# Kernel optimization log

Hardware: AMD Instinct MI355X
Metric: run time of the kernel (lower is better)

Reference implementation:

```python
import jax, jax.numpy as jnp
import numpy as np

B, T, N, C_IN, C_OUT, CHEB_K, ST_EMB = 8, 12, 2048, 64, 64, 2, 64


def setup_inputs() -> dict:
    key = jax.random.key(0)
    ks = jax.random.split(key, 9)
    inv = 1.0 / np.sqrt(ST_EMB)
    return {
        "x": jax.random.normal(ks[0], (B, T, N, C_IN), dtype=jnp.float32),
        "adj": jax.random.uniform(ks[1], (N, N), dtype=jnp.float32),
        "st_emb": jax.random.normal(ks[2], (T, 1, ST_EMB), dtype=jnp.float32),
        "weights": jax.random.normal(ks[3], (CHEB_K, C_IN, C_OUT), dtype=jnp.float32) * 0.02,
        "bias": jax.random.normal(ks[4], (C_OUT,), dtype=jnp.float32) * 0.02,
        "W1": jax.random.uniform(ks[5], (ST_EMB, 32), minval=-inv, maxval=inv, dtype=jnp.float32),
        "b1": jax.random.uniform(ks[6], (32,), minval=-inv, maxval=inv, dtype=jnp.float32),
        "W2": jax.random.uniform(ks[7], (32, 1), minval=-1/np.sqrt(32), maxval=1/np.sqrt(32), dtype=jnp.float32),
        "b2": jax.random.uniform(ks[8], (1,), minval=-1/np.sqrt(32), maxval=1/np.sqrt(32), dtype=jnp.float32),
    }


def reference(x, adj, st_emb, weights, bias, W1, b1, W2, b2):
    # lambda MLP: Linear -> ReLU -> Linear, then 1 + relu(.)
    h = jax.nn.relu(st_emb @ W1 + b1)            # [T,1,32]
    lam = 1.0 + jax.nn.relu(h @ W2 + b2)         # [T,1,1]
    c1 = (2.0 * lam - 2.0) / lam                 # [T,1,1] diagonal-scale coefficient
    c2 = 2.0 / lam                               # [T,1,1]
    # identity support einsum == per-time diagonal scaling of x
    x_g1 = c1[None] * x                          # [B,T,N,C]
    # adjacency support: scale factored out of the N x N contraction
    x_g2 = c2[None] * jnp.einsum('nm,btmc->btnc', adj, x)  # [B,T,N,C]
    x_g = jnp.stack([x_g1, x_g2], axis=3)        # [B,T,N,K,C]
    return jnp.einsum('btnki,kio->btno', x_g, weights) + bias
```

## Files before the change

kernel.cpp:

```cpp
#include <hip/hip_runtime.h>
#include <hip/hip_bf16.h>

#define B_ 8
#define T_ 12
#define N_ 2048
#define C_ 64
#define BM 128
#define BK 64

typedef __attribute__((ext_vector_type(4))) float f32x4;
typedef __attribute__((ext_vector_type(4))) __bf16 bf16x4;
typedef __attribute__((ext_vector_type(8))) __bf16 bf16x8;

#define GAS __attribute__((address_space(1)))
#define LAS __attribute__((address_space(3)))

static __device__ __forceinline__ void gld_lds16(const void* g, void* l) {
    __builtin_amdgcn_global_load_lds((const GAS void*)g, (LAS void*)l, 16, 0, 0);
}

#define WS_CBUF 0
#define WS_WTB  1024
#define WS_ADJB 32768
#define WS_XT   (32768 + 8388608)
#define WS_NEED ((size_t)(WS_XT) + 25165824)

__global__ void lam_kernel(const float* __restrict__ st, const float* __restrict__ W1,
                           const float* __restrict__ b1, const float* __restrict__ W2,
                           const float* __restrict__ b2, float* __restrict__ cbuf) {
    const int t = threadIdx.x >> 5;
    const int h = threadIdx.x & 31;
    if (t >= T_) return;
    float acc = b1[h];
    #pragma unroll 8
    for (int e = 0; e < 64; ++e) acc += st[t * 64 + e] * W1[e * 32 + h];
    float hv = fmaxf(acc, 0.f) * W2[h];
    #pragma unroll
    for (int off = 16; off; off >>= 1) hv += __shfl_down(hv, off, 32);
    if (h == 0) {
        float lam = 1.f + fmaxf(hv + b2[0], 0.f);
        cbuf[t]      = 2.f - 2.f / lam;
        cbuf[T_ + t] = 2.f / lam;
    }
}

__global__ void lamw_kernel(const float* __restrict__ st, const float* __restrict__ W1,
                            const float* __restrict__ b1, const float* __restrict__ W2,
                            const float* __restrict__ b2, const float* __restrict__ weights,
                            float* __restrict__ cbuf, __bf16* __restrict__ WtB) {
    const int t = threadIdx.x >> 5;
    const int h = threadIdx.x & 31;
    if (t < T_) {
        float acc = b1[h];
        #pragma unroll 8
        for (int e = 0; e < 64; ++e) acc += st[t * 64 + e] * W1[e * 32 + h];
        float hv = fmaxf(acc, 0.f) * W2[h];
        #pragma unroll
        for (int off = 16; off; off >>= 1) hv += __shfl_down(hv, off, 32);
        if (h == 0) {
            float lam = 1.f + fmaxf(hv + b2[0], 0.f);
            cbuf[t]      = 2.f - 2.f / lam;
            cbuf[T_ + t] = 2.f / lam;
        }
    }
    for (int e = threadIdx.x; e < 64 * 128; e += 512) {
        int o = e >> 7, k = e & 127;
        float v = (k < 64) ? weights[4096 + k * 64 + o] : weights[(k - 64) * 64 + o];
        WtB[o * 128 + k] = (__bf16)v;
    }
}

__global__ void cvt_adj(const float* __restrict__ adj, __bf16* __restrict__ adjb) {
    const int i = (blockIdx.x * 256 + threadIdx.x) * 8;
    const float4 f0 = *(const float4*)&adj[i];
    const float4 f1 = *(const float4*)&adj[i + 4];
    bf16x8 h = { (__bf16)f0.x, (__bf16)f0.y, (__bf16)f0.z, (__bf16)f0.w,
                 (__bf16)f1.x, (__bf16)f1.y, (__bf16)f1.z, (__bf16)f1.w };
    *(bf16x8*)&adjb[i] = h;
}

__global__ void cvt_x(const float* __restrict__ x, __bf16* __restrict__ xT) {
    __shared__ __align__(16) __bf16 t[64][72];
    const int bt = blockIdx.y, n0 = blockIdx.x * 64;
    const int tid = threadIdx.x;
    {
        const int r = tid >> 2, c0 = (tid & 3) * 16;
        const float* src = x + ((size_t)bt * N_ + n0 + r) * C_ + c0;
        #pragma unroll
        for (int i = 0; i < 4; ++i) {
            float4 f = *(const float4*)(src + 4 * i);
            t[c0 + 4 * i + 0][r] = (__bf16)f.x;
            t[c0 + 4 * i + 1][r] = (__bf16)f.y;
            t[c0 + 4 * i + 2][r] = (__bf16)f.z;
            t[c0 + 4 * i + 3][r] = (__bf16)f.w;
        }
    }
    __syncthreads();
    {
        const int c = tid >> 2, nf = (tid & 3) * 16;
        __bf16* dst = xT + ((size_t)bt * C_ + c) * N_ + n0 + nf;
        *(bf16x8*)(dst)     = *(const bf16x8*)&t[c][nf];
        *(bf16x8*)(dst + 8) = *(const bf16x8*)&t[c][nf + 8];
    }
}

__global__ __launch_bounds__(256, 3) void dgcn_main2(
    const __bf16* __restrict__ adjb, const __bf16* __restrict__ xT,
    const float* __restrict__ x, const __bf16* __restrict__ WtB,
    const float* __restrict__ bias, const float* __restrict__ cbuf,
    float* __restrict__ out)
{
    __shared__ __align__(16) __bf16 smem[24576];
    char* sb = (char*)smem;

    const int m0  = blockIdx.x * BM;
    const int btg = blockIdx.y;
    const int tid = threadIdx.x;
    const int l   = tid & 63, w = tid >> 6;
    const int wr  = w >> 1, wc = w & 1;
    const int lr  = l & 15, lk = l >> 4;

    #pragma unroll
    for (int i = 0; i < 4; ++i) {
        int s = (w * 4 + i) * 64 + l;
        int o = s >> 4, j = s & 15;
        *(bf16x8*)(sb + 32768 + s * 16) = *(const bf16x8*)(WtB + o * 128 + 8 * (j ^ (o & 7)));
    }

    const __bf16* srcA[4];
    const __bf16* srcB[4];
    #pragma unroll
    for (int i = 0; i < 4; ++i) {
        int s = (w * 4 + i) * 64 + l;
        int r = s >> 3, j = s & 7;
        srcA[i] = adjb + (size_t)(m0 + r) * N_ + 8 * (j ^ (r & 7));
        int bb = s >> 9, c = (s >> 3) & 63;
        srcB[i] = xT + ((size_t)(btg * 2 + bb) * C_ + c) * N_ + 8 * (j ^ (c & 7));
    }

    f32x4 acc[4][4] = {};

    for (int kt = 0; kt < N_ / BK; ++kt) {
        __syncthreads();
        #pragma unroll
        for (int i = 0; i < 4; ++i) {
            gld_lds16(srcA[i], sb + (w * 4 + i) * 1024);
            gld_lds16(srcB[i], sb + 16384 + (w * 4 + i) * 1024);
            srcA[i] += BK;
            srcB[i] += BK;
        }
        __syncthreads();
        #pragma unroll
        for (int ks = 0; ks < 2; ++ks) {
            const int kb = ks * 64 + lk * 16;
            bf16x8 a[4];
            #pragma unroll
            for (int mi = 0; mi < 4; ++mi) {
                int rr = wr * 64 + mi * 16 + lr;
                a[mi] = *(const bf16x8*)(sb + rr * 128 + (kb ^ ((rr & 7) << 4)));
            }
            #pragma unroll
            for (int nj = 0; nj < 4; ++nj) {
                int cc = nj * 16 + lr;
                bf16x8 b = *(const bf16x8*)(sb + 16384 + wc * 8192 + cc * 128 + (kb ^ ((cc & 7) << 4)));
                #pragma unroll
                for (int mi = 0; mi < 4; ++mi)
                    acc[mi][nj] = __builtin_amdgcn_mfma_f32_16x16x32_bf16(a[mi], b, acc[mi][nj], 0, 0, 0);
            }
        }
    }

    #pragma unroll
    for (int bb = 0; bb < 2; ++bb) {
        const int btA = btg * 2 + bb;
        const int tloc = btA % T_;
        const float c1 = cbuf[tloc];
        const float c2 = cbuf[T_ + tloc];
        __syncthreads();
        if (wc == bb) {
            #pragma unroll
            for (int mi = 0; mi < 4; ++mi)
                #pragma unroll
                for (int nj = 0; nj < 4; ++nj)
                    #pragma unroll
                    for (int q = 0; q < 4; ++q) {
                        int row = wr * 64 + mi * 16 + lk * 4 + q;
                        int colb = (nj * 16 + lr) * 2;
                        *(__bf16*)(sb + row * 256 + (colb ^ ((row & 7) << 4))) =
                            (__bf16)(c2 * acc[mi][nj][q]);
                    }
        }
        {
            int row = w * 32 + (l >> 1);
            int c0 = (l & 1) * 32;
            const float* xs = x + ((size_t)btA * N_ + m0 + row) * C_ + c0;
            #pragma unroll
            for (int i = 0; i < 4; ++i) {
                float4 f0 = *(const float4*)(xs + 8 * i);
                float4 f1 = *(const float4*)(xs + 8 * i + 4);
                bf16x8 h = { (__bf16)(c1 * f0.x), (__bf16)(c1 * f0.y),
                             (__bf16)(c1 * f0.z), (__bf16)(c1 * f0.w),
                             (__bf16)(c1 * f1.x), (__bf16)(c1 * f1.y),
                             (__bf16)(c1 * f1.z), (__bf16)(c1 * f1.w) };
                int colb = 128 + c0 * 2 + 16 * i;
                *(bf16x8*)(sb + row * 256 + (colb ^ ((row & 7) << 4))) = h;
            }
        }
        __syncthreads();
        f32x4 oacc[2][4] = {};
        #pragma unroll
        for (int ks = 0; ks < 4; ++ks) {
            const int kb = ks * 64 + lk * 16;
            bf16x8 ea[2];
            #pragma unroll
            for (int mi2 = 0; mi2 < 2; ++mi2) {
                int row = w * 32 + mi2 * 16 + lr;
                ea[mi2] = *(const bf16x8*)(sb + row * 256 + (kb ^ ((row & 7) << 4)));
            }
            #pragma unroll
            for (int nj = 0; nj < 4; ++nj) {
                int o = nj * 16 + lr;
                bf16x8 bw = *(const bf16x8*)(sb + 32768 + o * 256 + (kb ^ ((o & 7) << 4)));
                oacc[0][nj] = __builtin_amdgcn_mfma_f32_16x16x32_bf16(ea[0], bw, oacc[0][nj], 0, 0, 0);
                oacc[1][nj] = __builtin_amdgcn_mfma_f32_16x16x32_bf16(ea[1], bw, oacc[1][nj], 0, 0, 0);
            }
        }
        float* ob = out + (size_t)btA * N_ * C_;
        #pragma unroll
        for (int nj = 0; nj < 4; ++nj) {
            const float bv = bias[nj * 16 + lr];
            #pragma unroll
            for (int mi2 = 0; mi2 < 2; ++mi2)
                #pragma unroll
                for (int q = 0; q < 4; ++q) {
                    int row = w * 32 + mi2 * 16 + lk * 4 + q;
                    ob[(size_t)(m0 + row) * C_ + nj * 16 + lr] = oacc[mi2][nj][q] + bv;
                }
        }
    }
}

#define LDM 72
#define LDE 136
__global__ __launch_bounds__(256, 3) void dgcn_fb(
    const float* __restrict__ x, const float* __restrict__ adj,
    const float* __restrict__ weights, const float* __restrict__ bias,
    const float* __restrict__ cbuf, float* __restrict__ out)
{
    __shared__ __align__(16) __bf16 smem[BM * LDE];
    __shared__ __align__(16) __bf16 Wt[64 * LDE];
    __bf16* As = smem;
    __bf16* Bs = smem + BM * LDM;
    __bf16* E  = smem;

    const int mtile = blockIdx.x;
    const int bt    = blockIdx.y;
    const int tloc  = bt % T_;
    const int m0    = mtile * BM;
    const int tid   = threadIdx.x;
    const int lane  = tid & 63;
    const int w     = tid >> 6;

    const float c1 = cbuf[tloc];
    const float c2 = cbuf[T_ + tloc];
    const float* xbt = x + (size_t)bt * N_ * C_;

    for (int e = tid; e < 2 * 64 * 64; e += 256) {
        int kk = e >> 6, o = e & 63;
        float v = (kk < 64) ? weights[4096 + kk * 64 + o] : weights[(kk - 64) * 64 + o];
        Wt[o * LDE + kk] = (__bf16)v;
    }

    f32x4 acc[2][4] = {};
    const int c4 = tid & 15;
    const int rg = tid >> 4;
    const int lr = lane & 15;
    const int lk = lane >> 4;

    for (int kt = 0; kt < N_ / BK; ++kt) {
        const int k0 = kt * BK;
        __syncthreads();
        #pragma unroll
        for (int j = 0; j < 8; ++j) {
            const int r = rg + 16 * j;
            const float4 f = *(const float4*)&adj[(size_t)(m0 + r) * N_ + k0 + 4 * c4];
            bf16x4 h = { (__bf16)f.x, (__bf16)f.y, (__bf16)f.z, (__bf16)f.w };
            *(bf16x4*)&As[r * LDM + 4 * c4] = h;
        }
        #pragma unroll
        for (int j = 0; j < 4; ++j) {
            const int k  = (tid & 15) + 16 * j;
            const int c0 = 4 * (tid >> 4);
            const float4 f = *(const float4*)&xbt[(size_t)(k0 + k) * C_ + c0];
            Bs[(c0 + 0) * LDM + k] = (__bf16)f.x;
            Bs[(c0 + 1) * LDM + k] = (__bf16)f.y;
            Bs[(c0 + 2) * LDM + k] = (__bf16)f.z;
            Bs[(c0 + 3) * LDM + k] = (__bf16)f.w;
        }
        __syncthreads();
        #pragma unroll
        for (int ks = 0; ks < 2; ++ks) {
            bf16x8 a0 = *(const bf16x8*)&As[(w * 32 +  0 + lr) * LDM + ks * 32 + lk * 8];
            bf16x8 a1 = *(const bf16x8*)&As[(w * 32 + 16 + lr) * LDM + ks * 32 + lk * 8];
            #pragma unroll
            for (int nj = 0; nj < 4; ++nj) {
                bf16x8 b = *(const bf16x8*)&Bs[(nj * 16 + lr) * LDM + ks * 32 + lk * 8];
                acc[0][nj] = __builtin_amdgcn_mfma_f32_16x16x32_bf16(a0, b, acc[0][nj], 0, 0, 0);
                acc[1][nj] = __builtin_amdgcn_mfma_f32_16x16x32_bf16(a1, b, acc[1][nj], 0, 0, 0);
            }
        }
    }
    __syncthreads();

    #pragma unroll
    for (int j = 0; j < 8; ++j) {
        const int r = rg + 16 * j;
        const float4 f = *(const float4*)&xbt[(size_t)(m0 + r) * C_ + 4 * c4];
        bf16x4 h = { (__bf16)(c1 * f.x), (__bf16)(c1 * f.y), (__bf16)(c1 * f.z), (__bf16)(c1 * f.w) };
        *(bf16x4*)&E[r * LDE + 64 + 4 * c4] = h;
    }
    #pragma unroll
    for (int mi = 0; mi < 2; ++mi)
        #pragma unroll
        for (int nj = 0; nj < 4; ++nj)
            #pragma unroll
            for (int q = 0; q < 4; ++q) {
                const int row = w * 32 + mi * 16 + lk * 4 + q;
                const int col = nj * 16 + lr;
                E[row * LDE + col] = (__bf16)(c2 * acc[mi][nj][q]);
            }
    __syncthreads();

    f32x4 oacc[2][4] = {};
    #pragma unroll
    for (int ks = 0; ks < 4; ++ks) {
        bf16x8 a0 = *(const bf16x8*)&E[(w * 32 +  0 + lr) * LDE + ks * 32 + lk * 8];
        bf16x8 a1 = *(const bf16x8*)&E[(w * 32 + 16 + lr) * LDE + ks * 32 + lk * 8];
        #pragma unroll
        for (int nj = 0; nj < 4; ++nj) {
            bf16x8 bw = *(const bf16x8*)&Wt[(nj * 16 + lr) * LDE + ks * 32 + lk * 8];
            oacc[0][nj] = __builtin_amdgcn_mfma_f32_16x16x32_bf16(a0, bw, oacc[0][nj], 0, 0, 0);
            oacc[1][nj] = __builtin_amdgcn_mfma_f32_16x16x32_bf16(a1, bw, oacc[1][nj], 0, 0, 0);
        }
    }
    float* obt = out + (size_t)bt * N_ * C_;
    #pragma unroll
    for (int nj = 0; nj < 4; ++nj) {
        const float bv = bias[nj * 16 + lr];
        #pragma unroll
        for (int mi = 0; mi < 2; ++mi)
            #pragma unroll
            for (int q = 0; q < 4; ++q) {
                const int row = w * 32 + mi * 16 + lk * 4 + q;
                obt[(size_t)(m0 + row) * C_ + nj * 16 + lr] = oacc[mi][nj][q] + bv;
            }
    }
}

extern "C" void kernel_launch(void* const* d_in, const int* in_sizes, int n_in,
                              void* d_out, int out_size, void* d_ws, size_t ws_size,
                              hipStream_t stream) {
    const float* x       = (const float*)d_in[0];
    const float* adj     = (const float*)d_in[1];
    const float* st_emb  = (const float*)d_in[2];
    const float* weights = (const float*)d_in[3];
    const float* bias    = (const float*)d_in[4];
    const float* W1      = (const float*)d_in[5];
    const float* b1      = (const float*)d_in[6];
    const float* W2      = (const float*)d_in[7];
    const float* b2      = (const float*)d_in[8];
    float* out = (float*)d_out;
    char* ws = (char*)d_ws;
    float* cbuf = (float*)(ws + WS_CBUF);

    if (ws_size >= WS_NEED) {
        __bf16* WtB  = (__bf16*)(ws + WS_WTB);
        __bf16* adjb = (__bf16*)(ws + WS_ADJB);
        __bf16* xT   = (__bf16*)(ws + WS_XT);
        lamw_kernel<<<1, 512, 0, stream>>>(st_emb, W1, b1, W2, b2, weights, cbuf, WtB);
        cvt_adj<<<N_ * N_ / (256 * 8), 256, 0, stream>>>(adj, adjb);
        cvt_x<<<dim3(N_ / 64, B_ * T_), 256, 0, stream>>>(x, xT);
        dgcn_main2<<<dim3(N_ / BM, B_ * T_ / 2), 256, 0, stream>>>(adjb, xT, x, WtB, bias, cbuf, out);
    } else {
        lam_kernel<<<1, 384, 0, stream>>>(st_emb, W1, b1, W2, b2, cbuf);
        dgcn_fb<<<dim3(N_ / BM, B_ * T_), 256, 0, stream>>>(x, adj, weights, bias, cbuf, out);
    }
}
```

Before: 90.05 us.

## Double-buffer LDS tiles in main GEMM and fuse adj/x conversion kernels

The main adjacency GEMM now double-buffers its LDS tiles: the next K-tile's async global-to-LDS loads are issued before computing on the current buffer, which removes one barrier per iteration and overlaps loads with MFMA work. LDS grows from 48KB to 64KB, so launch bounds drop to 2 blocks per CU and the output weights are read straight from global memory instead of being staged in LDS. The two conversion kernels for adj and x are merged into a single launch to cut launch overhead. A single barrier per iteration with async LDS loads may leave a write-after-read hazard unless the wait semantics cover it, and occupancy is lower.

```diff
diff --git a/kernel.cpp b/kernel.cpp
--- a/kernel.cpp
+++ b/kernel.cpp
@@ -70,19 +70,21 @@
     }
 }
 
-__global__ void cvt_adj(const float* __restrict__ adj, __bf16* __restrict__ adjb) {
-    const int i = (blockIdx.x * 256 + threadIdx.x) * 8;
-    const float4 f0 = *(const float4*)&adj[i];
-    const float4 f1 = *(const float4*)&adj[i + 4];
-    bf16x8 h = { (__bf16)f0.x, (__bf16)f0.y, (__bf16)f0.z, (__bf16)f0.w,
-                 (__bf16)f1.x, (__bf16)f1.y, (__bf16)f1.z, (__bf16)f1.w };
-    *(bf16x8*)&adjb[i] = h;
-}
-
-__global__ void cvt_x(const float* __restrict__ x, __bf16* __restrict__ xT) {
+__global__ void cvt_fused(const float* __restrict__ x, __bf16* __restrict__ xT,
+                          const float* __restrict__ adj, __bf16* __restrict__ adjb) {
+    const int bid = blockIdx.x;
+    const int tid = threadIdx.x;
+    if (bid >= 3072) {
+        const size_t i = ((size_t)(bid - 3072) * 256 + tid) * 8;
+        const float4 f0 = *(const float4*)&adj[i];
+        const float4 f1 = *(const float4*)&adj[i + 4];
+        bf16x8 h = { (__bf16)f0.x, (__bf16)f0.y, (__bf16)f0.z, (__bf16)f0.w,
+                     (__bf16)f1.x, (__bf16)f1.y, (__bf16)f1.z, (__bf16)f1.w };
+        *(bf16x8*)&adjb[i] = h;
+        return;
+    }
     __shared__ __align__(16) __bf16 t[64][72];
-    const int bt = blockIdx.y, n0 = blockIdx.x * 64;
-    const int tid = threadIdx.x;
+    const int bt = bid >> 5, n0 = (bid & 31) * 64;
     {
         const int r = tid >> 2, c0 = (tid & 3) * 16;
         const float* src = x + ((size_t)bt * N_ + n0 + r) * C_ + c0;
@@ -104,13 +106,13 @@
     }
 }
 
-__global__ __launch_bounds__(256, 3) void dgcn_main2(
+__global__ __launch_bounds__(256, 2) void dgcn_main2(
     const __bf16* __restrict__ adjb, const __bf16* __restrict__ xT,
     const float* __restrict__ x, const __bf16* __restrict__ WtB,
     const float* __restrict__ bias, const float* __restrict__ cbuf,
     float* __restrict__ out)
 {
-    __shared__ __align__(16) __bf16 smem[24576];
+    __shared__ __align__(16) __bf16 smem[32768];
     char* sb = (char*)smem;
 
     const int m0  = blockIdx.x * BM;
@@ -120,13 +122,6 @@
     const int wr  = w >> 1, wc = w & 1;
     const int lr  = l & 15, lk = l >> 4;
 
-    #pragma unroll
-    for (int i = 0; i < 4; ++i) {
-        int s = (w * 4 + i) * 64 + l;
-        int o = s >> 4, j = s & 15;
-        *(bf16x8*)(sb + 32768 + s * 16) = *(const bf16x8*)(WtB + o * 128 + 8 * (j ^ (o & 7)));
-    }
-
     const __bf16* srcA[4];
     const __bf16* srcB[4];
     #pragma unroll
@@ -140,16 +135,26 @@
 
     f32x4 acc[4][4] = {};
 
+    #pragma unroll
+    for (int i = 0; i < 4; ++i) {
+        gld_lds16(srcA[i], sb + (w * 4 + i) * 1024);
+        gld_lds16(srcB[i], sb + 16384 + (w * 4 + i) * 1024);
+    }
+
+    int sel = 0;
     for (int kt = 0; kt < N_ / BK; ++kt) {
         __syncthreads();
-        #pragma unroll
-        for (int i = 0; i < 4; ++i) {
-            gld_lds16(srcA[i], sb + (w * 4 + i) * 1024);
-            gld_lds16(srcB[i], sb + 16384 + (w * 4 + i) * 1024);
-            srcA[i] += BK;
-            srcB[i] += BK;
-        }
-        __syncthreads();
+        if (kt < N_ / BK - 1) {
+            const int wo = (sel ^ 1) * 32768;
+            #pragma unroll
+            for (int i = 0; i < 4; ++i) {
+                srcA[i] += BK;
+                srcB[i] += BK;
+                gld_lds16(srcA[i], sb + wo + (w * 4 + i) * 1024);
+                gld_lds16(srcB[i], sb + wo + 16384 + (w * 4 + i) * 1024);
+            }
+        }
+        const char* base = sb + sel * 32768;
         #pragma unroll
         for (int ks = 0; ks < 2; ++ks) {
             const int kb = ks * 64 + lk * 16;
@@ -157,17 +162,18 @@
             #pragma unroll
             for (int mi = 0; mi < 4; ++mi) {
                 int rr = wr * 64 + mi * 16 + lr;
-                a[mi] = *(const bf16x8*)(sb + rr * 128 + (kb ^ ((rr & 7) << 4)));
+                a[mi] = *(const bf16x8*)(base + rr * 128 + (kb ^ ((rr & 7) << 4)));
             }
             #pragma unroll
             for (int nj = 0; nj < 4; ++nj) {
                 int cc = nj * 16 + lr;
-                bf16x8 b = *(const bf16x8*)(sb + 16384 + wc * 8192 + cc * 128 + (kb ^ ((cc & 7) << 4)));
+                bf16x8 b = *(const bf16x8*)(base + 16384 + wc * 8192 + cc * 128 + (kb ^ ((cc & 7) << 4)));
                 #pragma unroll
                 for (int mi = 0; mi < 4; ++mi)
                     acc[mi][nj] = __builtin_amdgcn_mfma_f32_16x16x32_bf16(a[mi], b, acc[mi][nj], 0, 0, 0);
             }
         }
+        sel ^= 1;
     }
 
     #pragma unroll
@@ -220,7 +226,7 @@
             #pragma unroll
             for (int nj = 0; nj < 4; ++nj) {
                 int o = nj * 16 + lr;
-                bf16x8 bw = *(const bf16x8*)(sb + 32768 + o * 256 + (kb ^ ((o & 7) << 4)));
+                bf16x8 bw = *(const bf16x8*)(WtB + o * 128 + ks * 32 + lk * 8);
                 oacc[0][nj] = __builtin_amdgcn_mfma_f32_16x16x32_bf16(ea[0], bw, oacc[0][nj], 0, 0, 0);
                 oacc[1][nj] = __builtin_amdgcn_mfma_f32_16x16x32_bf16(ea[1], bw, oacc[1][nj], 0, 0, 0);
             }
@@ -378,8 +384,7 @@
         __bf16* adjb = (__bf16*)(ws + WS_ADJB);
         __bf16* xT   = (__bf16*)(ws + WS_XT);
         lamw_kernel<<<1, 512, 0, stream>>>(st_emb, W1, b1, W2, b2, weights, cbuf, WtB);
-        cvt_adj<<<N_ * N_ / (256 * 8), 256, 0, stream>>>(adj, adjb);
-        cvt_x<<<dim3(N_ / 64, B_ * T_), 256, 0, stream>>>(x, xT);
+        cvt_fused<<<5120, 256, 0, stream>>>(x, xT, adj, adjb);
         dgcn_main2<<<dim3(N_ / BM, B_ * T_ / 2), 256, 0, stream>>>(adjb, xT, x, WtB, bias, cbuf, out);
     } else {
         lam_kernel<<<1, 384, 0, stream>>>(st_emb, W1, b1, W2, b2, cbuf);
```

Result: slower. 99.15 us (+10.1%).
